# Kernel optimization log

Hardware: AMD Instinct MI355X
Metric: run time of the kernel (lower is better)

The kernel has to match this reference:

```python
import jax, jax.numpy as jnp
import numpy as np

ALPHA = 4.0          # spikingjelly default surrogate.Sigmoid(alpha=4.0)
V_TH = 1.0           # IFNode default v_threshold
BN_EPS = 1e-5

@jax.custom_vjp
def spike(x):
    # heaviside forward
    return (x >= 0.0).astype(x.dtype)

def _spike_fwd(x):
    return spike(x), x

def _spike_bwd(x, g):
    s = jax.nn.sigmoid(ALPHA * x)
    return (g * ALPHA * s * (1.0 - s),)

spike.defvjp(_spike_fwd, _spike_bwd)

def if_node(x_seq):
    """Multi-step IF neuron: integrate, threshold, hard reset (v_reset=0),
    detach_reset=True. x_seq: [T, ...] -> spikes [T, ...]."""
    def step(v, xt):
        v = v + xt
        s = spike(v - V_TH)
        v = v * (1.0 - jax.lax.stop_gradient(s))  # detached hard reset to 0
        return v, s
    _, s_seq = jax.lax.scan(step, jnp.zeros_like(x_seq[0]), x_seq)
    return s_seq

def bn1d(x, gamma, beta):
    """Training-mode BatchNorm1d over flattened (T*B) batch dim. x: [T,B,F]."""
    m = x.mean(axis=(0, 1))
    v = x.var(axis=(0, 1))  # biased variance, matches torch normalization
    return (x - m) * jax.lax.rsqrt(v + BN_EPS) * gamma + beta

def setup_inputs() -> dict:
    key = jax.random.key(0)
    ks = jax.random.split(key, 12)
    T, B, C, H, W = 8, 64, 2, 128, 128
    F0, D, NC = C * H * W, 2048, 1000
    x = jax.random.uniform(ks[0], (T, B, C, H, W), dtype=jnp.float32)
    def kaiming(k, out_f, in_f):
        # kaiming_normal_ mode='fan_out', relu gain: std = sqrt(2/out_f)
        return jax.random.normal(k, (out_f, in_f), dtype=jnp.float32) * np.sqrt(2.0 / out_f)
    def bias(k, out_f, in_f):
        bound = 1.0 / np.sqrt(in_f)
        return jax.random.uniform(k, (out_f,), dtype=jnp.float32, minval=-bound, maxval=bound)
    inp = {"x": x}
    dims = [(D, F0), (D, D), (D, D)]
    for i, (o, f) in enumerate(dims):
        inp[f"W{i}"] = kaiming(ks[1 + i], o, f)
        inp[f"b{i}"] = bias(ks[4 + i], o, f)
        inp[f"g{i}"] = jnp.ones((o,), jnp.float32)
        inp[f"be{i}"] = jnp.zeros((o,), jnp.float32)
    inp["Wout"] = kaiming(ks[7], NC, D)
    inp["bout"] = bias(ks[8], NC, D)
    return inp

def reference(x, W0, b0, g0, be0, W1, b1, g1, be1, W2, b2, g2, be2, Wout, bout):
    T, B = x.shape[0], x.shape[1]
    h = x.reshape(T, B, -1)           # [T,B,32768]
    h = if_node(h)                    # sn0
    for Wl, bl, gl, bel in ((W0, b0, g0, be0), (W1, b1, g1, be1), (W2, b2, g2, be2)):
        h = jnp.einsum('tbi,oi->tbo', h, Wl) + bl
        h = bn1d(h, gl, bel)
        h = if_node(h)
    out = jnp.einsum('tbi,oi->tbo', h, Wout) + bout  # [T,B,1000]
    return out.mean(axis=0)           # [B,1000]
```

## Files before the change

### kernel.cpp

```cpp
#include <hip/hip_runtime.h>


#define T_STEPS 8
#define BATCH 64
#define F0 32768
#define DIM 2048
#define NROWS 512
#define NC 1000

typedef __attribute__((ext_vector_type(8))) short short8;
typedef __attribute__((ext_vector_type(4))) float f32x4;

__device__ __forceinline__ unsigned short bf16_rne(float f) {
    unsigned int u = __float_as_uint(f);
    u += 0x7FFFu + ((u >> 16) & 1u);
    return (unsigned short)(u >> 16);
}

#define BM 256
#define BN 256
#define BK 64

#define SBAR() do { __builtin_amdgcn_sched_barrier(0); \
                    __builtin_amdgcn_s_barrier();      \
                    __builtin_amdgcn_sched_barrier(0); } while (0)

__device__ __forceinline__ short8 lds_frag(const unsigned short* base, int row, int kb) {
    const int off = row * 128 + (kb ^ ((row & 7) << 4));
    return *(const short8*)((const char*)base + off);
}

__global__ __launch_bounds__(512) void gemm_splitk(
    const unsigned short* __restrict__ A, const float* __restrict__ W,
    float* __restrict__ part, int M, int N, int K, int Kpart, int Wrows)
{
    __shared__ unsigned short As[2][BM * BK];
    __shared__ unsigned short Hs[BN * BK];
    __shared__ unsigned short Ls[BN * BK];

    const int gx = gridDim.x, gy = gridDim.y;
    const int nwg = gx * gy * gridDim.z;
    const int lid = blockIdx.x + gx * (blockIdx.y + gy * blockIdx.z);
    const int cpx = nwg >> 3;
    const int nid = (lid & 7) * cpx + (lid >> 3);
    const int bx  = nid % gx;
    const int by  = (nid / gx) % gy;
    const int kz  = nid / (gx * gy);

    const int tid  = threadIdx.x;
    const int lane = tid & 63;
    const int w    = tid >> 6;
    const int bm   = bx * BM;
    const int bn   = by * BN;
    const int ksteps = Kpart / BK;
    const int wm = (w >> 2) * 128;
    const int wn = (w & 3) * 64;
    const int kbase = kz * Kpart;

    f32x4 acc[8][4] = {};
    float4 wv[8];

    auto issue_loads = [&](int buf, int kt) {
        const int k0 = kbase + kt * BK;
#pragma unroll
        for (int i = 0; i < 8; ++i) {
            const int n  = (tid >> 4) + 32 * i;
            const int c4 = tid & 15;
            const int gn = min(bn + n, Wrows - 1);
            wv[i] = *(const float4*)&W[(size_t)gn * K + k0 + c4 * 4];
        }
#pragma unroll
        for (int c = 0; c < 4; ++c) {
            const int r    = c * 64 + w * 8 + (lane >> 3);
            const int colb = ((lane & 7) * 16) ^ ((r & 7) << 4);
            const char* src = (const char*)A + ((size_t)(bm + r) * K + k0) * 2 + colb;
            unsigned short* dst = &As[buf][(c * 64 + w * 8) * BK];
            __builtin_amdgcn_global_load_lds(
                (const __attribute__((address_space(1))) void*)src,
                (__attribute__((address_space(3))) void*)dst, 16, 0, 0);
        }
    };

    auto convert_write = [&]() {
#pragma unroll
        for (int i = 0; i < 8; ++i) {
            const int n  = (tid >> 4) + 32 * i;
            const int c4 = tid & 15;
            const float vf[4] = {wv[i].x, wv[i].y, wv[i].z, wv[i].w};
            unsigned short h[4], l[4];
#pragma unroll
            for (int e = 0; e < 4; ++e) {
                h[e] = bf16_rne(vf[e]);
                const float hf = __uint_as_float((unsigned int)h[e] << 16);
                l[e] = bf16_rne(vf[e] - hf);
            }
            const int off = n * 128 + ((c4 * 8) ^ ((n & 7) << 4));
            *(ushort4*)((char*)Hs + off) = make_ushort4(h[0], h[1], h[2], h[3]);
            *(ushort4*)((char*)Ls + off) = make_ushort4(l[0], l[1], l[2], l[3]);
        }
    };

    issue_loads(0, 0);
    convert_write();
    asm volatile("s_waitcnt vmcnt(0) lgkmcnt(0)" ::: "memory");
    SBAR();

    int cur = 0;
    for (int kt = 0; kt < ksteps; ++kt) {
        const bool last = (kt + 1 == ksteps);
        if (!last) issue_loads(cur ^ 1, kt + 1);

#pragma unroll
        for (int kk = 0; kk < 2; ++kk) {
            const int kb = (kk * 32 + (lane >> 4) * 8) * 2;
            short8 bh[4], bl[4];
#pragma unroll
            for (int i = 0; i < 4; ++i) {
                const int r = wn + i * 16 + (lane & 15);
                bh[i] = lds_frag(Hs, r, kb);
                bl[i] = lds_frag(Ls, r, kb);
            }
#pragma unroll
            for (int mi = 0; mi < 8; ++mi) {
                const short8 a = lds_frag(&As[cur][0], wm + mi * 16 + (lane & 15), kb);
#pragma unroll
                for (int ni = 0; ni < 4; ++ni) {
                    acc[mi][ni] = __builtin_amdgcn_mfma_f32_16x16x32_bf16(
                        a, bh[ni], acc[mi][ni], 0, 0, 0);
                    acc[mi][ni] = __builtin_amdgcn_mfma_f32_16x16x32_bf16(
                        a, bl[ni], acc[mi][ni], 0, 0, 0);
                }
            }
        }

        if (!last) {
            SBAR();
            convert_write();
            asm volatile("s_waitcnt vmcnt(0) lgkmcnt(0)" ::: "memory");
            SBAR();
            cur ^= 1;
        }
    }

    const size_t zoff = (size_t)kz * M * N;
#pragma unroll
    for (int mi = 0; mi < 8; ++mi) {
        const int gr0 = bm + wm + mi * 16 + (lane >> 4) * 4;
#pragma unroll
        for (int ni = 0; ni < 4; ++ni) {
            const int gc = bn + wn + ni * 16 + (lane & 15);
            if (gc < N) {
#pragma unroll
                for (int e = 0; e < 4; ++e) {
                    const int gr = gr0 + e;
                    if (gr < M) part[zoff + (size_t)gr * N + gc] = acc[mi][ni][e];
                }
            }
        }
    }
}

__global__ __launch_bounds__(256) void reduce_bias(
    const float* __restrict__ part, const float* __restrict__ bias,
    float* __restrict__ out, int KS, int MN, int N)
{
    const int i4 = blockIdx.x * 256 + threadIdx.x;
    if (i4 * 4 >= MN) return;
    float4 s = make_float4(0.f, 0.f, 0.f, 0.f);
    for (int z = 0; z < KS; ++z) {
        const float4 p = *(const float4*)&part[(size_t)z * MN + i4 * 4];
        s.x += p.x; s.y += p.y; s.z += p.z; s.w += p.w;
    }
    const int col = (i4 * 4) % N;
    const float4 b = *(const float4*)&bias[col];
    s.x += b.x; s.y += b.y; s.z += b.z; s.w += b.w;
    *(float4*)&out[(size_t)i4 * 4] = s;
}

__global__ __launch_bounds__(256) void if0_kernel(
    const float* __restrict__ x, unsigned short* __restrict__ s)
{
    const size_t id4 = ((size_t)blockIdx.x * 256 + threadIdx.x) * 4;
    float v0 = 0.f, v1 = 0.f, v2 = 0.f, v3 = 0.f;
#pragma unroll
    for (int t = 0; t < T_STEPS; ++t) {
        const size_t idx = (size_t)t * (BATCH * (size_t)F0) + id4;
        const float4 xv = *(const float4*)&x[idx];
        ushort4 o;
        v0 += xv.x; if (v0 >= 1.f) { o.x = 0x3F80; v0 = 0.f; } else o.x = 0;
        v1 += xv.y; if (v1 >= 1.f) { o.y = 0x3F80; v1 = 0.f; } else o.y = 0;
        v2 += xv.z; if (v2 >= 1.f) { o.z = 0x3F80; v2 = 0.f; } else o.z = 0;
        v3 += xv.w; if (v3 >= 1.f) { o.w = 0x3F80; v3 = 0.f; } else o.w = 0;
        *(ushort4*)&s[idx] = o;
    }
}

__global__ __launch_bounds__(256) void bn_stats_if(
    const float* __restrict__ z, const float* __restrict__ g,
    const float* __restrict__ be, unsigned short* __restrict__ s)
{
    __shared__ float ssum[4][64], ssq[4][64];
    __shared__ float ssc[64], ssh[64];
    const int l = threadIdx.x & 63;
    const int q = threadIdx.x >> 6;
    const int f = blockIdx.x * 64 + l;
    float sum = 0.f, sq = 0.f;
    for (int r = q; r < NROWS; r += 4) {
        const float v = z[(size_t)r * DIM + f];
        sum += v; sq += v * v;
    }
    ssum[q][l] = sum; ssq[q][l] = sq;
    __syncthreads();
    if (threadIdx.x < 64) {
        float ts = 0.f, tq = 0.f;
#pragma unroll
        for (int i = 0; i < 4; ++i) { ts += ssum[i][l]; tq += ssq[i][l]; }
        const float mean = ts * (1.0f / NROWS);
        const float var  = tq * (1.0f / NROWS) - mean * mean;
        const float inv  = rsqrtf(var + 1e-5f);
        const float sc   = g[f] * inv;
        ssc[l] = sc;
        ssh[l] = be[f] - mean * sc;
    }
    __syncthreads();
    const float sc = ssc[l];
    const float sh = ssh[l];
    for (int b = q; b < BATCH; b += 4) {
        const int id = b * DIM + f;
        float v = 0.f;
#pragma unroll
        for (int t = 0; t < T_STEPS; ++t) {
            const size_t idx = (size_t)t * (BATCH * DIM) + id;
            v += z[idx] * sc + sh;
            if (v >= 1.0f) { s[idx] = 0x3F80; v = 0.f; }
            else           { s[idx] = 0; }
        }
    }
}

__global__ __launch_bounds__(256) void bn_stats_if_mean(
    const float* __restrict__ z, const float* __restrict__ g,
    const float* __restrict__ be, unsigned short* __restrict__ sbar)
{
    __shared__ float ssum[4][64], ssq[4][64];
    __shared__ float ssc[64], ssh[64];
    const int l = threadIdx.x & 63;
    const int q = threadIdx.x >> 6;
    const int f = blockIdx.x * 64 + l;
    float sum = 0.f, sq = 0.f;
    for (int r = q; r < NROWS; r += 4) {
        const float v = z[(size_t)r * DIM + f];
        sum += v; sq += v * v;
    }
    ssum[q][l] = sum; ssq[q][l] = sq;
    __syncthreads();
    if (threadIdx.x < 64) {
        float ts = 0.f, tq = 0.f;
#pragma unroll
        for (int i = 0; i < 4; ++i) { ts += ssum[i][l]; tq += ssq[i][l]; }
        const float mean = ts * (1.0f / NROWS);
        const float var  = tq * (1.0f / NROWS) - mean * mean;
        const float inv  = rsqrtf(var + 1e-5f);
        const float sc   = g[f] * inv;
        ssc[l] = sc;
        ssh[l] = be[f] - mean * sc;
    }
    __syncthreads();
    const float sc = ssc[l];
    const float sh = ssh[l];
    for (int b = q; b < BATCH; b += 4) {
        const int id = b * DIM + f;
        float v = 0.f;
        int cnt = 0;
#pragma unroll
        for (int t = 0; t < T_STEPS; ++t) {
            const size_t idx = (size_t)t * (BATCH * DIM) + id;
            v += z[idx] * sc + sh;
            if (v >= 1.0f) { cnt++; v = 0.f; }
        }
        sbar[id] = bf16_rne((float)cnt * 0.125f);
    }
}

extern "C" void kernel_launch(void* const* d_in, const int* in_sizes, int n_in,
                              void* d_out, int out_size, void* d_ws, size_t ws_size,
                              hipStream_t stream)
{
    const float* x    = (const float*)d_in[0];
    const float* W0   = (const float*)d_in[1];
    const float* b0   = (const float*)d_in[2];
    const float* g0   = (const float*)d_in[3];
    const float* be0  = (const float*)d_in[4];
    const float* W1   = (const float*)d_in[5];
    const float* b1   = (const float*)d_in[6];
    const float* g1   = (const float*)d_in[7];
    const float* be1  = (const float*)d_in[8];
    const float* W2   = (const float*)d_in[9];
    const float* b2   = (const float*)d_in[10];
    const float* g2   = (const float*)d_in[11];
    const float* be2  = (const float*)d_in[12];
    const float* Wout = (const float*)d_in[13];
    const float* bout = (const float*)d_in[14];
    float* out = (float*)d_out;
    (void)in_sizes; (void)n_in; (void)out_size; (void)ws_size;

    char* ws = (char*)d_ws;
    size_t off = 0;
    auto alloc = [&](size_t nbytes) {
        char* p = ws + off;
        off = (off + nbytes + 255) & ~(size_t)255;
        return p;
    };
    unsigned short* s0 = (unsigned short*)alloc((size_t)NROWS * F0 * 2);
    unsigned short* s1 = (unsigned short*)alloc((size_t)NROWS * DIM * 2);
    unsigned short* s2 = (unsigned short*)alloc((size_t)NROWS * DIM * 2);
    unsigned short* sb = (unsigned short*)alloc((size_t)256 * DIM * 2);
    float* z    = (float*)alloc((size_t)NROWS * DIM * 4);
    float* part = (float*)alloc((size_t)16 * NROWS * DIM * 4);

    const int MN = NROWS * DIM;

    if0_kernel<<<(BATCH * (size_t)F0) / 4 / 256, 256, 0, stream>>>(x, s0);

    gemm_splitk<<<dim3(NROWS / BM, DIM / BN, 16), 512, 0, stream>>>(
        s0, W0, part, NROWS, DIM, F0, F0 / 16, DIM);
    reduce_bias<<<MN / 4 / 256, 256, 0, stream>>>(part, b0, z, 16, MN, DIM);
    bn_stats_if<<<DIM / 64, 256, 0, stream>>>(z, g0, be0, s1);

    gemm_splitk<<<dim3(NROWS / BM, DIM / BN, 16), 512, 0, stream>>>(
        s1, W1, part, NROWS, DIM, DIM, DIM / 16, DIM);
    reduce_bias<<<MN / 4 / 256, 256, 0, stream>>>(part, b1, z, 16, MN, DIM);
    bn_stats_if<<<DIM / 64, 256, 0, stream>>>(z, g1, be1, s2);

    gemm_splitk<<<dim3(NROWS / BM, DIM / BN, 16), 512, 0, stream>>>(
        s2, W2, part, NROWS, DIM, DIM, DIM / 16, DIM);
    reduce_bias<<<MN / 4 / 256, 256, 0, stream>>>(part, b2, z, 16, MN, DIM);
    bn_stats_if_mean<<<DIM / 64, 256, 0, stream>>>(z, g2, be2, sb);

    gemm_splitk<<<dim3(1, (NC + BN - 1) / BN, 16), 512, 0, stream>>>(
        sb, Wout, part, BATCH, NC, DIM, DIM / 16, NC);
    reduce_bias<<<(BATCH * NC / 4 + 255) / 256, 256, 0, stream>>>(
        part, bout, out, 16, BATCH * NC, NC);
}
```

Measured before the change: 428.7 us.

## Pipeline split-K GEMM with double-buffered bf16 hi/lo W tiles and BK=32

Restructures the split-K GEMM main loop into a deeper software pipeline. W loads run two steps ahead in two register sets, and the bf16 hi/lo converted W tiles are double-buffered in LDS, so conversion overlaps with MFMA on the other buffer and one barrier per step is removed. BK drops to 32 with a new swizzle, conversion uses v_cvt_pk_bf16_f32 and packed rounding, and s_setprio raises wave priority during MFMA. The smaller K-step means more loop iterations and barriers, and the partial vmcnt waits must match the load order exactly.

```diff
diff --git a/kernel.cpp b/kernel.cpp
--- a/kernel.cpp
+++ b/kernel.cpp
@@ -19,24 +19,19 @@
 
 #define BM 256
 #define BN 256
-#define BK 64
+#define BK 32
 
 #define SBAR() do { __builtin_amdgcn_sched_barrier(0); \
                     __builtin_amdgcn_s_barrier();      \
                     __builtin_amdgcn_sched_barrier(0); } while (0)
 
-__device__ __forceinline__ short8 lds_frag(const unsigned short* base, int row, int kb) {
-    const int off = row * 128 + (kb ^ ((row & 7) << 4));
-    return *(const short8*)((const char*)base + off);
-}
-
 __global__ __launch_bounds__(512) void gemm_splitk(
     const unsigned short* __restrict__ A, const float* __restrict__ W,
     float* __restrict__ part, int M, int N, int K, int Kpart, int Wrows)
 {
     __shared__ unsigned short As[2][BM * BK];
-    __shared__ unsigned short Hs[BN * BK];
-    __shared__ unsigned short Ls[BN * BK];
+    __shared__ unsigned short Hs[2][BN * BK];
+    __shared__ unsigned short Ls[2][BN * BK];
 
     const int gx = gridDim.x, gy = gridDim.y;
     const int nwg = gx * gy * gridDim.z;
@@ -50,96 +45,116 @@
     const int tid  = threadIdx.x;
     const int lane = tid & 63;
     const int w    = tid >> 6;
+    const int l15  = lane & 15;
     const int bm   = bx * BM;
     const int bn   = by * BN;
-    const int ksteps = Kpart / BK;
-    const int wm = (w >> 2) * 128;
-    const int wn = (w & 3) * 64;
+    const int ks   = Kpart / BK;
+    const int wm   = (w >> 2) * 128;
+    const int wn   = (w & 3) * 64;
     const int kbase = kz * Kpart;
 
     f32x4 acc[8][4] = {};
-    float4 wv[8];
-
-    auto issue_loads = [&](int buf, int kt) {
+    float4 wv0[4], wv1[4];
+
+    auto issueA = [&](int buf, int kt) {
         const int k0 = kbase + kt * BK;
-#pragma unroll
-        for (int i = 0; i < 8; ++i) {
-            const int n  = (tid >> 4) + 32 * i;
-            const int c4 = tid & 15;
-            const int gn = min(bn + n, Wrows - 1);
-            wv[i] = *(const float4*)&W[(size_t)gn * K + k0 + c4 * 4];
-        }
-#pragma unroll
-        for (int c = 0; c < 4; ++c) {
-            const int r    = c * 64 + w * 8 + (lane >> 3);
-            const int colb = ((lane & 7) * 16) ^ ((r & 7) << 4);
+        const int colb = ((lane & 3) ^ ((lane >> 2) & 3)) << 4;
+#pragma unroll
+        for (int c = 0; c < 2; ++c) {
+            const int r = w * 32 + c * 16 + (lane >> 2);
             const char* src = (const char*)A + ((size_t)(bm + r) * K + k0) * 2 + colb;
-            unsigned short* dst = &As[buf][(c * 64 + w * 8) * BK];
+            unsigned short* dst = &As[buf][(w * 32 + c * 16) * BK];
             __builtin_amdgcn_global_load_lds(
                 (const __attribute__((address_space(1))) void*)src,
                 (__attribute__((address_space(3))) void*)dst, 16, 0, 0);
         }
     };
-
-    auto convert_write = [&]() {
-#pragma unroll
-        for (int i = 0; i < 8; ++i) {
-            const int n  = (tid >> 4) + 32 * i;
-            const int c4 = tid & 15;
-            const float vf[4] = {wv[i].x, wv[i].y, wv[i].z, wv[i].w};
-            unsigned short h[4], l[4];
-#pragma unroll
-            for (int e = 0; e < 4; ++e) {
-                h[e] = bf16_rne(vf[e]);
-                const float hf = __uint_as_float((unsigned int)h[e] << 16);
-                l[e] = bf16_rne(vf[e] - hf);
+    auto issueW = [&](float4* wv, int kt) {
+        const int k0 = kbase + kt * BK;
+#pragma unroll
+        for (int i = 0; i < 4; ++i) {
+            const int q  = tid + 512 * i;
+            const int n  = q >> 3;
+            const int c4 = q & 7;
+            const int gn = min(bn + n, Wrows - 1);
+            wv[i] = *(const float4*)&W[(size_t)gn * K + k0 + c4 * 4];
+        }
+    };
+    auto convertW = [&](const float4* wv, int buf) {
+#pragma unroll
+        for (int i = 0; i < 4; ++i) {
+            const int q  = tid + 512 * i;
+            const int n  = q >> 3;
+            const int c4 = q & 7;
+            const unsigned u0 = __float_as_uint(wv[i].x);
+            const unsigned u1 = __float_as_uint(wv[i].y);
+            const unsigned u2 = __float_as_uint(wv[i].z);
+            const unsigned u3 = __float_as_uint(wv[i].w);
+            const unsigned r0 = (u0 + 0x7FFFu + ((u0 >> 16) & 1u)) & 0xFFFF0000u;
+            const unsigned r1 = (u1 + 0x7FFFu + ((u1 >> 16) & 1u)) & 0xFFFF0000u;
+            const unsigned r2 = (u2 + 0x7FFFu + ((u2 >> 16) & 1u)) & 0xFFFF0000u;
+            const unsigned r3 = (u3 + 0x7FFFu + ((u3 >> 16) & 1u)) & 0xFFFF0000u;
+            const unsigned hi01 = (r0 >> 16) | r1;
+            const unsigned hi23 = (r2 >> 16) | r3;
+            const float l0 = wv[i].x - __uint_as_float(r0);
+            const float l1 = wv[i].y - __uint_as_float(r1);
+            const float l2 = wv[i].z - __uint_as_float(r2);
+            const float l3 = wv[i].w - __uint_as_float(r3);
+            unsigned lo01, lo23;
+            asm("v_cvt_pk_bf16_f32 %0, %1, %2" : "=v"(lo01) : "v"(l0), "v"(l1));
+            asm("v_cvt_pk_bf16_f32 %0, %1, %2" : "=v"(lo23) : "v"(l2), "v"(l3));
+            const int off = n * 64 + ((((c4 >> 1) ^ (n & 3)) << 4) | ((c4 & 1) * 8));
+            *(uint2*)((char*)&Hs[buf][0] + off) = make_uint2(hi01, hi23);
+            *(uint2*)((char*)&Ls[buf][0] + off) = make_uint2(lo01, lo23);
+        }
+    };
+    auto mfmaStep = [&](int ab, int hb) {
+        __builtin_amdgcn_s_setprio(1);
+        short8 bh[4], bl[4];
+#pragma unroll
+        for (int i = 0; i < 4; ++i) {
+            const int r = wn + i * 16 + l15;
+            const int po = r * 64 + (((lane >> 4) ^ (r & 3)) << 4);
+            bh[i] = *(const short8*)((const char*)&Hs[hb][0] + po);
+            bl[i] = *(const short8*)((const char*)&Ls[hb][0] + po);
+        }
+#pragma unroll
+        for (int mi = 0; mi < 8; ++mi) {
+            const int r = wm + mi * 16 + l15;
+            const short8 a = *(const short8*)(
+                (const char*)&As[ab][0] + r * 64 + (((lane >> 4) ^ (r & 3)) << 4));
+#pragma unroll
+            for (int ni = 0; ni < 4; ++ni) {
+                acc[mi][ni] = __builtin_amdgcn_mfma_f32_16x16x32_bf16(
+                    a, bh[ni], acc[mi][ni], 0, 0, 0);
+                acc[mi][ni] = __builtin_amdgcn_mfma_f32_16x16x32_bf16(
+                    a, bl[ni], acc[mi][ni], 0, 0, 0);
             }
-            const int off = n * 128 + ((c4 * 8) ^ ((n & 7) << 4));
-            *(ushort4*)((char*)Hs + off) = make_ushort4(h[0], h[1], h[2], h[3]);
-            *(ushort4*)((char*)Ls + off) = make_ushort4(l[0], l[1], l[2], l[3]);
-        }
-    };
-
-    issue_loads(0, 0);
-    convert_write();
-    asm volatile("s_waitcnt vmcnt(0) lgkmcnt(0)" ::: "memory");
+        }
+        __builtin_amdgcn_s_setprio(0);
+    };
+
+    issueW(wv0, 0);
+    issueA(0, 0);
+    issueW(wv1, (1 < ks) ? 1 : 0);
+    convertW(wv0, 0);
+    asm volatile("s_waitcnt vmcnt(4) lgkmcnt(0)" ::: "memory");
     SBAR();
 
-    int cur = 0;
-    for (int kt = 0; kt < ksteps; ++kt) {
-        const bool last = (kt + 1 == ksteps);
-        if (!last) issue_loads(cur ^ 1, kt + 1);
-
-#pragma unroll
-        for (int kk = 0; kk < 2; ++kk) {
-            const int kb = (kk * 32 + (lane >> 4) * 8) * 2;
-            short8 bh[4], bl[4];
-#pragma unroll
-            for (int i = 0; i < 4; ++i) {
-                const int r = wn + i * 16 + (lane & 15);
-                bh[i] = lds_frag(Hs, r, kb);
-                bl[i] = lds_frag(Ls, r, kb);
-            }
-#pragma unroll
-            for (int mi = 0; mi < 8; ++mi) {
-                const short8 a = lds_frag(&As[cur][0], wm + mi * 16 + (lane & 15), kb);
-#pragma unroll
-                for (int ni = 0; ni < 4; ++ni) {
-                    acc[mi][ni] = __builtin_amdgcn_mfma_f32_16x16x32_bf16(
-                        a, bh[ni], acc[mi][ni], 0, 0, 0);
-                    acc[mi][ni] = __builtin_amdgcn_mfma_f32_16x16x32_bf16(
-                        a, bl[ni], acc[mi][ni], 0, 0, 0);
-                }
-            }
-        }
-
-        if (!last) {
-            SBAR();
-            convert_write();
-            asm volatile("s_waitcnt vmcnt(0) lgkmcnt(0)" ::: "memory");
-            SBAR();
-            cur ^= 1;
-        }
+    for (int t = 0; t < ks; t += 2) {
+        if (t + 1 < ks) issueA(1, t + 1);
+        issueW(wv0, min(t + 2, ks - 1));
+        mfmaStep(0, 0);
+        if (t + 1 < ks) convertW(wv1, 1);
+        asm volatile("s_waitcnt vmcnt(4) lgkmcnt(0)" ::: "memory");
+        SBAR();
+        if (t + 1 >= ks) break;
+        if (t + 2 < ks) issueA(0, t + 2);
+        issueW(wv1, min(t + 3, ks - 1));
+        mfmaStep(1, 1);
+        if (t + 2 < ks) convertW(wv0, 0);
+        asm volatile("s_waitcnt vmcnt(4) lgkmcnt(0)" ::: "memory");
+        SBAR();
     }
 
     const size_t zoff = (size_t)kz * M * N;
@@ -148,7 +163,7 @@
         const int gr0 = bm + wm + mi * 16 + (lane >> 4) * 4;
 #pragma unroll
         for (int ni = 0; ni < 4; ++ni) {
-            const int gc = bn + wn + ni * 16 + (lane & 15);
+            const int gc = bn + wn + ni * 16 + l15;
             if (gc < N) {
 #pragma unroll
                 for (int e = 0; e < 4; ++e) {
```

After: 1.116 ms. 2.6x slower.
